# Kernel tuning notes

Hardware: AMD Instinct MI355X
Metric: run time of the kernel (lower is better)

## Reference

```python
import jax, jax.numpy as jnp
import numpy as np

B, LATENT, HID, OUT, SEQ = 256, 512, 1024, 256, 128


def setup_inputs() -> dict:
    key = jax.random.key(0)
    ks = jax.random.split(key, 5)
    s = lambda fan: 1.0 / np.sqrt(fan)
    return {
        "latent": jax.random.normal(ks[0], (B, LATENT), jnp.float32),
        "fc_W": jax.random.normal(ks[1], (HID, LATENT), jnp.float32) * s(LATENT),
        "fc_b": jnp.zeros((HID,), jnp.float32),
        "W_ih": jax.random.normal(ks[2], (4 * HID, OUT), jnp.float32) * s(HID),
        "W_hh": jax.random.normal(ks[3], (4 * HID, HID), jnp.float32) * s(HID),
        "b_ih": jnp.zeros((4 * HID,), jnp.float32),
        "b_hh": jnp.zeros((4 * HID,), jnp.float32),
        "out_W": jax.random.normal(ks[4], (OUT, HID), jnp.float32) * s(HID),
        "out_b": jnp.zeros((OUT,), jnp.float32),
    }


def reference(latent, fc_W, fc_b, W_ih, W_hh, b_ih, b_hh, out_W, out_b):
    # hidden init from latent; cell init zero (num_layers = 1)
    h0 = latent @ fc_W.T + fc_b                       # [B, HID]
    c0 = jnp.zeros_like(h0)
    x0 = jnp.zeros((latent.shape[0], out_W.shape[0]), latent.dtype)  # [B, OUT]
    bias = b_ih + b_hh
    H = h0.shape[-1]

    def step(carry, _):
        x, h, c = carry
        gates = x @ W_ih.T + h @ W_hh.T + bias        # [B, 4H], torch order i,f,g,o
        i = jax.nn.sigmoid(gates[:, 0 * H:1 * H])
        f = jax.nn.sigmoid(gates[:, 1 * H:2 * H])
        g = jnp.tanh(gates[:, 2 * H:3 * H])
        o = jax.nn.sigmoid(gates[:, 3 * H:4 * H])
        c = f * c + i * g
        h = o * jnp.tanh(c)
        y = h @ out_W.T + out_b                        # [B, OUT]; fed back as next input
        return (y, h, c), y

    _, ys = jax.lax.scan(step, (x0, h0, c0), None, length=SEQ)
    return jnp.transpose(ys, (1, 0, 2))               # [B, SEQ, OUT]
```

## Files before the change

### kernel.cpp

```cpp
#include <hip/hip_runtime.h>


typedef __attribute__((ext_vector_type(8))) _Float16 f16x8;
typedef __attribute__((ext_vector_type(4))) float f32x4;
typedef __attribute__((ext_vector_type(4))) unsigned u32x4;

#define MFMA16(a,b,c) __builtin_amdgcn_mfma_f32_16x16x32_f16(a,b,c,0,0,0)

__device__ __forceinline__ short f2h(float x){
  return __builtin_bit_cast(short, (_Float16)x);
}
__device__ __forceinline__ unsigned pack2h(float a, float b){
  unsigned short ua = __builtin_bit_cast(unsigned short, (_Float16)a);
  unsigned short ub = __builtin_bit_cast(unsigned short, (_Float16)b);
  return (unsigned)ua | ((unsigned)ub << 16);
}

__device__ __forceinline__ void gll16(const void* g, void* l){
  __builtin_amdgcn_global_load_lds((const __attribute__((address_space(1))) void*)g,
                                   (__attribute__((address_space(3))) void*)l, 16, 0, 0);
}

__device__ __forceinline__ void stage_t(const short* gRC, int ldk, short* lds, int lane, int wv){
#pragma unroll
  for (int jj = 0; jj < 2; ++jj){
    int j = wv*2 + jj;
    const short* src = gRC + (size_t)(j*8 + (lane>>3))*ldk + ((lane&7)*8);
    gll16(src, lds + j*512);
  }
}

__device__ __forceinline__ f16x8 fragh(const short* t, int r, int kk, int lane){
  int row = r + (lane & 15);
  int k0  = (kk<<5) + ((lane>>4)<<3);
  return *(const f16x8*)(t + row*64 + (k0 ^ ((row & 7)<<3)));
}

template<int CH>
__device__ __forceinline__ void core_k(const short* Ag, const short* Bg, int ldk,
                                       short* As, short* Bs, f32x4 (&acc)[2][2],
                                       int lane, int wv, int wr, int wc){
  stage_t(Ag, ldk, As, lane, wv);
  stage_t(Bg, ldk, Bs, lane, wv);
  __syncthreads();
  int buf = 0;
  for (int c = 0; c < CH; ++c){
    if (c+1 < CH){
      stage_t(Ag + (c+1)*64, ldk, As + (buf^1)*4096, lane, wv);
      stage_t(Bg + (c+1)*64, ldk, Bs + (buf^1)*4096, lane, wv);
    }
    const short* At = As + buf*4096;
    const short* Bt = Bs + buf*4096;
#pragma unroll
    for (int kk = 0; kk < 2; ++kk){
      f16x8 a0 = fragh(At, wr,    kk, lane), a1 = fragh(At, wr+16, kk, lane);
      f16x8 b0 = fragh(Bt, wc,    kk, lane), b1 = fragh(Bt, wc+16, kk, lane);
      acc[0][0] = MFMA16(a0,b0,acc[0][0]); acc[0][1] = MFMA16(a0,b1,acc[0][1]);
      acc[1][0] = MFMA16(a1,b0,acc[1][0]); acc[1][1] = MFMA16(a1,b1,acc[1][1]);
    }
    __syncthreads();
    buf ^= 1;
  }
}


__global__ void k_prep(const float* __restrict__ W_ih, const float* __restrict__ out_W,
                       const float* __restrict__ latent, const float* __restrict__ fc_W,
                       const float* __restrict__ W_hh,
                       const float* __restrict__ b_ih, const float* __restrict__ b_hh,
                       short* __restrict__ WihF, short* __restrict__ owT,
                       short* __restrict__ owB, short* __restrict__ latF,
                       short* __restrict__ fcwF, short* __restrict__ W0F,
                       float* __restrict__ bias0, unsigned* __restrict__ flags){
  int T = blockDim.x*gridDim.x, t0 = blockIdx.x*blockDim.x + threadIdx.x;
  for (int i = t0; i < 8192; i += T) flags[i] = 0u;
  for (int idx = t0; idx < 4096*256; idx += T){
    int r = idx >> 8, j = idx & 255;
    WihF[(size_t)r*256 + (j ^ ((r&7)<<3))] = f2h(W_ih[idx]);
  }
  for (int idx = t0; idx < 1024*256; idx += T){
    int c = idx >> 8, j = idx & 255;
    owT[(size_t)c*256 + (j ^ ((c&7)<<3))] = f2h(out_W[(size_t)j*1024 + c]);
  }
  for (int idx = t0; idx < 256*1024; idx += T){
    int o = idx >> 10, k = idx & 1023;
    owB[(size_t)o*1024 + (k ^ ((o&7)<<3))] = f2h(out_W[idx]);
  }
  for (int idx = t0; idx < 256*512; idx += T){
    int b = idx >> 9, j = idx & 511;
    latF[(size_t)b*512 + (j ^ ((b&7)<<3))] = f2h(latent[idx]);
  }
  for (int idx = t0; idx < 1024*512; idx += T){
    int n = idx >> 9, j = idx & 511;
    fcwF[(size_t)n*512 + (j ^ ((n&7)<<3))] = f2h(fc_W[idx]);
  }
  for (int idx = t0; idx < 4096*1024; idx += T){
    int r = idx >> 10, k = idx & 1023;
    int p = ((r & 1023)<<2) | (r >> 10);
    size_t a = ((size_t)(p>>4)*32 + (k>>5))*512 + ((size_t)((((k>>3)&3)<<4)|(p&15)))*8 + (k&7);
    W0F[a] = f2h(W_hh[idx]);
  }
  for (int r = t0; r < 4096; r += T){
    int rp = ((r & 1023)<<2) | (r >> 10);
    bias0[rp] = b_ih[r] + b_hh[r];
  }
}

__global__ void k_bias1(const float* __restrict__ W_ih, const float* __restrict__ out_b,
                        const float* __restrict__ bias0, float* __restrict__ bias1){
  int r = blockIdx.x*256 + threadIdx.x;
  float s = 0.f;
  for (int j = 0; j < 256; ++j) s += W_ih[(size_t)r*256 + j]*out_b[j];
  int rp = ((r & 1023)<<2) | (r >> 10);
  bias1[rp] = bias0[rp] + s;
}

__global__ __launch_bounds__(256) void k_wtotal(const short* __restrict__ WihF,
                                                const short* __restrict__ owT,
                                                const float* __restrict__ W_hh,
                                                short* __restrict__ WtF){
  __shared__ __align__(16) short As[2*4096];
  __shared__ __align__(16) short Bs[2*4096];
  int tid = threadIdx.x, lane = tid & 63, wv = tid >> 6;
  int wr = (wv>>1)*32, wc = (wv&1)*32;
  int Rm = blockIdx.x*64, Rn = blockIdx.y*64;
  f32x4 acc[2][2] = {};
  core_k<4>(WihF + (size_t)Rm*256, owT + (size_t)Rn*256, 256, As, Bs, acc, lane, wv, wr, wc);
#pragma unroll
  for (int mi = 0; mi < 2; ++mi)
#pragma unroll
  for (int ni = 0; ni < 2; ++ni)
#pragma unroll
  for (int r = 0; r < 4; ++r){
    int row = Rm + wr + mi*16 + ((lane>>4)<<2) + r;
    int col = Rn + wc + ni*16 + (lane & 15);
    float v = acc[mi][ni][r] + W_hh[(size_t)row*1024 + col];
    int p = ((row & 1023)<<2) | (row >> 10);
    size_t a = ((size_t)(p>>4)*32 + (col>>5))*512 + ((size_t)((((col>>3)&3)<<4)|(p&15)))*8 + (col&7);
    WtF[a] = f2h(v);
  }
}

__global__ __launch_bounds__(256) void k_h0(const short* __restrict__ latF,
                                            const short* __restrict__ fcwF,
                                            const float* __restrict__ fc_b,
                                            short* __restrict__ A0){
  __shared__ __align__(16) short As[2*4096];
  __shared__ __align__(16) short Bs[2*4096];
  int tid = threadIdx.x, lane = tid & 63, wv = tid >> 6;
  int wr = (wv>>1)*32, wc = (wv&1)*32;
  int Rm = blockIdx.x*64, Rn = blockIdx.y*64;
  f32x4 acc[2][2] = {};
  core_k<8>(latF + (size_t)Rm*512, fcwF + (size_t)Rn*512, 512, As, Bs, acc, lane, wv, wr, wc);
#pragma unroll
  for (int mi = 0; mi < 2; ++mi)
#pragma unroll
  for (int ni = 0; ni < 2; ++ni)
#pragma unroll
  for (int r = 0; r < 4; ++r){
    int row = Rm + wr + mi*16 + ((lane>>4)<<2) + r;
    int col = Rn + wc + ni*16 + (lane & 15);
    float h = acc[mi][ni][r] + fc_b[col];
    A0[(size_t)row*1024 + (col ^ ((row&7)<<3))] = f2h(h);
  }
}

__global__ __launch_bounds__(512, 1) void k_persist(
    const short* __restrict__ WtF, const short* __restrict__ W0F,
    const float* __restrict__ bias0, const float* __restrict__ bias1,
    short* __restrict__ A0, short* __restrict__ A1, short* __restrict__ Hh,
    unsigned* __restrict__ flags){
  __shared__ __align__(16) short Asl[32*1024];
  __shared__ __align__(16) float Lg0[32*132];
  __shared__ __align__(16) float Lg1[32*132];
  const int tid = threadIdx.x, lane = tid & 63, wv = tid >> 6;
  const int wg = blockIdx.x;
  const int chain = wg & 7, gw = wg >> 3;
  const int wn = wv & 3, kh = wv >> 2;
  const int cbase = gw*8 + wn*2, sbase = kh*16;

  f16x8 Breg[2][16];
  {
    const short* src = WtF + ((size_t)cbase*32 + sbase)*512 + lane*8;
#pragma unroll
    for (int cf = 0; cf < 2; ++cf)
#pragma unroll
      for (int s = 0; s < 16; ++s)
        Breg[cf][s] = *(const f16x8*)(src + (size_t)(cf*32 + s)*512);
  }
  const short* W0base = W0F + ((size_t)cbase*32 + sbase)*512 + lane*8;

  const int r0 = lane & 15;
  const int kql = (lane>>4)<<3;
  const int sw = (r0 & 7) << 3;

  const int er = tid >> 4, up = tid & 15;
  const int grow = chain*32 + er;
  const int swE = (grow & 7) << 3;
  const int posE = (gw*32 + 2*up) ^ swE;
  const f32x4 b1qA = *(const f32x4*)(bias1 + gw*128 + 8*up);
  const f32x4 b1qB = *(const f32x4*)(bias1 + gw*128 + 8*up + 4);
  float cA = 0.f, cB = 0.f;

  unsigned* flagC = flags + (size_t)chain*64;

  for (int t = 0; t < 128; ++t){
    const short* Ain = (t & 1) ? A1 : A0;
    short* Aout = (t & 1) ? A0 : A1;

    {
      u32x4 stg[8];
      const short* base = Ain + (size_t)(chain*32)*1024;
#pragma unroll
      for (int q = 0; q < 8; ++q){
        int i = wv*8 + q;
        const short* src = base + (size_t)(i>>1)*1024 + (i&1)*512 + lane*8;
        asm volatile("global_load_dwordx4 %0, %1, off sc0 sc1"
                     : "=v"(stg[q]) : "v"(src));
      }
      asm volatile("s_waitcnt vmcnt(0)" ::: "memory");
#pragma unroll
      for (int q = 0; q < 8; ++q){
        int i = wv*8 + q;
        *(u32x4*)((char*)Asl + (size_t)i*1024 + (size_t)lane*16) = stg[q];
      }
    }
    __syncthreads();

    f32x4 acc[2][2] = {};
    const short* Ar0 = Asl + r0*1024;
    const short* Ar1 = Asl + (16 + r0)*1024;
    if (t == 0){
#pragma unroll
      for (int s = 0; s < 16; ++s){
        int k = (sbase + s)*32 + kql;
        f16x8 w0 = *(const f16x8*)(W0base + (size_t)(0*32 + s)*512);
        f16x8 w1 = *(const f16x8*)(W0base + (size_t)(1*32 + s)*512);
        f16x8 a0 = *(const f16x8*)(Ar0 + (k ^ sw));
        f16x8 a1 = *(const f16x8*)(Ar1 + (k ^ sw));
        acc[0][0] = MFMA16(a0, w0, acc[0][0]);
        acc[0][1] = MFMA16(a0, w1, acc[0][1]);
        acc[1][0] = MFMA16(a1, w0, acc[1][0]);
        acc[1][1] = MFMA16(a1, w1, acc[1][1]);
      }
    } else {
#pragma unroll
      for (int s = 0; s < 16; ++s){
        int k = (sbase + s)*32 + kql;
        f16x8 a0 = *(const f16x8*)(Ar0 + (k ^ sw));
        f16x8 a1 = *(const f16x8*)(Ar1 + (k ^ sw));
        acc[0][0] = MFMA16(a0, Breg[0][s], acc[0][0]);
        acc[0][1] = MFMA16(a0, Breg[1][s], acc[0][1]);
        acc[1][0] = MFMA16(a1, Breg[0][s], acc[1][0]);
        acc[1][1] = MFMA16(a1, Breg[1][s], acc[1][1]);
      }
    }
    {
      float* Lg = kh ? Lg1 : Lg0;
#pragma unroll
      for (int rf = 0; rf < 2; ++rf)
#pragma unroll
      for (int cf = 0; cf < 2; ++cf)
#pragma unroll
      for (int j = 0; j < 4; ++j)
        Lg[(rf*16 + ((lane>>4)<<2) + j)*132 + wn*32 + cf*16 + r0] = acc[rf][cf][j];
    }
    __syncthreads();
    {
      f32x4 gA = *(const f32x4*)(Lg0 + er*132 + 8*up);
      f32x4 gB = *(const f32x4*)(Lg0 + er*132 + 8*up + 4);
      f32x4 hA = *(const f32x4*)(Lg1 + er*132 + 8*up);
      f32x4 hB = *(const f32x4*)(Lg1 + er*132 + 8*up + 4);
      if (t){ gA = gA + hA + b1qA; gB = gB + hB + b1qB; }
      else {
        gA = gA + hA + *(const f32x4*)(bias0 + gw*128 + 8*up);
        gB = gB + hB + *(const f32x4*)(bias0 + gw*128 + 8*up + 4);
      }
      float I0 = 1.f/(1.f+__expf(-gA[0])), F0 = 1.f/(1.f+__expf(-gA[1]));
      float G0 = tanhf(gA[2]),             O0 = 1.f/(1.f+__expf(-gA[3]));
      float I1 = 1.f/(1.f+__expf(-gB[0])), F1 = 1.f/(1.f+__expf(-gB[1]));
      float G1 = tanhf(gB[2]),             O1 = 1.f/(1.f+__expf(-gB[3]));
      cA = F0*cA + I0*G0;  float h0v = O0*tanhf(cA);
      cB = F1*cB + I1*G1;  float h1v = O1*tanhf(cB);
      unsigned pk = pack2h(h0v, h1v);
      short* pa = Aout + (size_t)grow*1024 + posE;
      asm volatile("global_store_dword %0, %1, off sc0 sc1" :: "v"(pa), "v"(pk));
      *(unsigned*)(Hh + (size_t)t*262144 + (size_t)grow*1024 + posE) = pk;
      asm volatile("s_waitcnt vmcnt(0)" ::: "memory");
    }
    if (t < 127){
      __syncthreads();
      if (tid == 0){
        unsigned val = (unsigned)(t+1);
        unsigned* fp = flagC + gw;
        asm volatile("global_store_dword %0, %1, off sc0 sc1" :: "v"(fp), "v"(val) : "memory");
      }
      if (wv == 0){
        const unsigned* pp = flagC + (size_t)lane*4;
        unsigned tgt = (unsigned)(t+1);
        while (true){
          u32x4 f;
          asm volatile("global_load_dwordx4 %0, %1, off sc0 sc1\n\ts_waitcnt vmcnt(0)"
                       : "=v"(f) : "v"(pp) : "memory");
          bool ok = (lane >= 8) || (f[0] >= tgt && f[1] >= tgt && f[2] >= tgt && f[3] >= tgt);
          if (__all(ok)) break;
        }
      }
      __syncthreads();
    }
  }
}

__global__ __launch_bounds__(512) void k_y(const short* __restrict__ Hh,
                                           const short* __restrict__ owB,
                                           const float* __restrict__ out_b,
                                           float* __restrict__ out){
  __shared__ __align__(16) short As[2*8192];
  __shared__ __align__(16) short Bs[2*16384];
  int tid = threadIdx.x, lane = tid & 63, wv = tid >> 6;
  int wr = (wv>>2)*64, wc = (wv&3)*64;
  size_t Rm = (size_t)blockIdx.x * 128;
  const short* Ab = Hh + Rm*1024;
  f32x4 acc[4][4] = {};
  auto stA = [&](int c, short* dst){
#pragma unroll
    for (int jj = 0; jj < 2; ++jj){ int j = wv*2 + jj;
      gll16(Ab + (size_t)(j*8 + (lane>>3))*1024 + c*64 + (lane&7)*8, dst + j*512); }
  };
  auto stB = [&](int c, short* dst){
#pragma unroll
    for (int jj = 0; jj < 4; ++jj){ int j = wv*4 + jj;
      gll16(owB + (size_t)(j*8 + (lane>>3))*1024 + c*64 + (lane&7)*8, dst + j*512); }
  };
  stA(0, As); stB(0, Bs);
  __syncthreads();
  int buf = 0;
  for (int c = 0; c < 16; ++c){
    if (c+1 < 16){ stA(c+1, As + (buf^1)*8192); stB(c+1, Bs + (buf^1)*16384); }
    const short* At = As + buf*8192;
    const short* Bt = Bs + buf*16384;
#pragma unroll
    for (int kk = 0; kk < 2; ++kk){
      f16x8 av[4], bv[4];
#pragma unroll
      for (int mi = 0; mi < 4; ++mi) av[mi] = fragh(At, wr + mi*16, kk, lane);
#pragma unroll
      for (int ni = 0; ni < 4; ++ni) bv[ni] = fragh(Bt, wc + ni*16, kk, lane);
#pragma unroll
      for (int mi = 0; mi < 4; ++mi)
#pragma unroll
      for (int ni = 0; ni < 4; ++ni) acc[mi][ni] = MFMA16(av[mi], bv[ni], acc[mi][ni]);
    }
    __syncthreads();
    buf ^= 1;
  }
#pragma unroll
  for (int ni = 0; ni < 4; ++ni){
    int col = wc + ni*16 + (lane & 15);
    float bv = out_b[col];
#pragma unroll
    for (int mi = 0; mi < 4; ++mi)
#pragma unroll
    for (int r = 0; r < 4; ++r){
      size_t m = Rm + wr + mi*16 + ((lane>>4)<<2) + r;
      int t = (int)(m >> 8), bb = (int)(m & 255);
      out[(size_t)bb*32768 + (size_t)t*256 + col] = acc[mi][ni][r] + bv;
    }
  }
}

extern "C" void kernel_launch(void* const* d_in, const int* in_sizes, int n_in,
                              void* d_out, int out_size, void* d_ws, size_t ws_size,
                              hipStream_t stream) {
  (void)in_sizes; (void)n_in; (void)out_size; (void)ws_size;
  const float* latent = (const float*)d_in[0];
  const float* fc_W   = (const float*)d_in[1];
  const float* fc_b   = (const float*)d_in[2];
  const float* W_ih   = (const float*)d_in[3];
  const float* W_hh   = (const float*)d_in[4];
  const float* b_ih   = (const float*)d_in[5];
  const float* b_hh   = (const float*)d_in[6];
  const float* out_W  = (const float*)d_in[7];
  const float* out_b  = (const float*)d_in[8];
  float* out = (float*)d_out;
  char*  ws  = (char*)d_ws;
  const size_t MB = 1u << 20;
  short* WtF   = (short*)(ws + 0);
  short* W0F   = (short*)(ws + 8*MB);
  short* A0    = (short*)(ws + 16*MB);
  short* A1    = (short*)(ws + 16*MB + 524288);
  float* bias0 = (float*)(ws + 17*MB);
  float* bias1 = (float*)(ws + 17*MB + 65536);
  short* owB   = (short*)(ws + 17*MB + 131072);
  short* WihF  = (short*)(ws + 18*MB);
  short* owT   = (short*)(ws + 20*MB);
  short* latF  = (short*)(ws + 20*MB + 524288);
  short* fcwF  = (short*)(ws + 21*MB);
  unsigned* flg= (unsigned*)(ws + 22*MB);
  short* Hh    = (short*)(ws + 23*MB);

  k_prep<<<1024, 256, 0, stream>>>(W_ih, out_W, latent, fc_W, W_hh, b_ih, b_hh,
                                   WihF, owT, owB, latF, fcwF, W0F, bias0, flg);
  k_bias1<<<16, 256, 0, stream>>>(W_ih, out_b, bias0, bias1);
  k_wtotal<<<dim3(64,16), 256, 0, stream>>>(WihF, owT, W_hh, WtF);
  k_h0<<<dim3(4,16), 256, 0, stream>>>(latF, fcwF, fc_b, A0);
  k_persist<<<256, 512, 0, stream>>>(WtF, W0F, bias0, bias1, A0, A1, Hh, flg);
  k_y<<<256, 512, 0, stream>>>(Hh, owB, out_b, out);
}
```

Before: 655.1 us.

## Read recurrent state from Hh history and stage it via direct global-to-LDS loads

Drops the A0/A1 ping-pong buffers. Each step now stores h once to the Hh history slice with a coherent store, and the next step reads that slice back, which removes one global store per thread per step. The A-tile staging is switched from register loads plus LDS writes to global_load_lds, and the resident weights are loaded with inline asm after an acquire fence. A risk is coherence: global_load_lds is issued without the sc0/sc1 bits, so it may read stale cached data from other workgroups unless the flag handshake and fence are enough, and no explicit vmcnt wait is visible before the barrier.

```diff
diff --git a/kernel.cpp b/kernel.cpp
--- a/kernel.cpp
+++ b/kernel.cpp
@@ -20,6 +20,8 @@
   __builtin_amdgcn_global_load_lds((const __attribute__((address_space(1))) void*)g,
                                    (__attribute__((address_space(3))) void*)l, 16, 0, 0);
 }
+
+__device__ __forceinline__ void vm0(){ asm volatile("s_waitcnt vmcnt(0)" ::: "memory"); }
 
 __device__ __forceinline__ void stage_t(const short* gRC, int ldk, short* lds, int lane, int wv){
 #pragma unroll
@@ -168,7 +170,7 @@
 __global__ __launch_bounds__(512, 1) void k_persist(
     const short* __restrict__ WtF, const short* __restrict__ W0F,
     const float* __restrict__ bias0, const float* __restrict__ bias1,
-    short* __restrict__ A0, short* __restrict__ A1, short* __restrict__ Hh,
+    const short* __restrict__ A0, short* __restrict__ Hh,
     unsigned* __restrict__ flags){
   __shared__ __align__(16) short Asl[32*1024];
   __shared__ __align__(16) float Lg0[32*132];
@@ -179,14 +181,19 @@
   const int wn = wv & 3, kh = wv >> 2;
   const int cbase = gw*8 + wn*2, sbase = kh*16;
 
-  f16x8 Breg[2][16];
+  __builtin_amdgcn_fence(__ATOMIC_ACQUIRE, "agent");
+
+  u32x4 braw[2][16];
   {
     const short* src = WtF + ((size_t)cbase*32 + sbase)*512 + lane*8;
 #pragma unroll
     for (int cf = 0; cf < 2; ++cf)
 #pragma unroll
-      for (int s = 0; s < 16; ++s)
-        Breg[cf][s] = *(const f16x8*)(src + (size_t)(cf*32 + s)*512);
+      for (int s = 0; s < 16; ++s){
+        const short* p = src + (size_t)(cf*32 + s)*512;
+        asm volatile("global_load_dwordx4 %0, %1, off" : "=v"(braw[cf][s]) : "v"(p));
+      }
+    vm0();
   }
   const short* W0base = W0F + ((size_t)cbase*32 + sbase)*512 + lane*8;
 
@@ -205,24 +212,13 @@
   unsigned* flagC = flags + (size_t)chain*64;
 
   for (int t = 0; t < 128; ++t){
-    const short* Ain = (t & 1) ? A1 : A0;
-    short* Aout = (t & 1) ? A0 : A1;
-
     {
-      u32x4 stg[8];
-      const short* base = Ain + (size_t)(chain*32)*1024;
+      const short* base = (t == 0) ? A0 : (Hh + (size_t)(t-1)*262144);
+      const short* bb = base + (size_t)(chain*32)*1024;
 #pragma unroll
       for (int q = 0; q < 8; ++q){
         int i = wv*8 + q;
-        const short* src = base + (size_t)(i>>1)*1024 + (i&1)*512 + lane*8;
-        asm volatile("global_load_dwordx4 %0, %1, off sc0 sc1"
-                     : "=v"(stg[q]) : "v"(src));
-      }
-      asm volatile("s_waitcnt vmcnt(0)" ::: "memory");
-#pragma unroll
-      for (int q = 0; q < 8; ++q){
-        int i = wv*8 + q;
-        *(u32x4*)((char*)Asl + (size_t)i*1024 + (size_t)lane*16) = stg[q];
+        gll16(bb + (size_t)(i>>1)*1024 + (i&1)*512 + lane*8, Asl + i*512);
       }
     }
     __syncthreads();
@@ -249,10 +245,10 @@
         int k = (sbase + s)*32 + kql;
         f16x8 a0 = *(const f16x8*)(Ar0 + (k ^ sw));
         f16x8 a1 = *(const f16x8*)(Ar1 + (k ^ sw));
-        acc[0][0] = MFMA16(a0, Breg[0][s], acc[0][0]);
-        acc[0][1] = MFMA16(a0, Breg[1][s], acc[0][1]);
-        acc[1][0] = MFMA16(a1, Breg[0][s], acc[1][0]);
-        acc[1][1] = MFMA16(a1, Breg[1][s], acc[1][1]);
+        acc[0][0] = MFMA16(a0, __builtin_bit_cast(f16x8, braw[0][s]), acc[0][0]);
+        acc[0][1] = MFMA16(a0, __builtin_bit_cast(f16x8, braw[1][s]), acc[0][1]);
+        acc[1][0] = MFMA16(a1, __builtin_bit_cast(f16x8, braw[0][s]), acc[1][0]);
+        acc[1][1] = MFMA16(a1, __builtin_bit_cast(f16x8, braw[1][s]), acc[1][1]);
       }
     }
     {
@@ -283,10 +279,9 @@
       cA = F0*cA + I0*G0;  float h0v = O0*tanhf(cA);
       cB = F1*cB + I1*G1;  float h1v = O1*tanhf(cB);
       unsigned pk = pack2h(h0v, h1v);
-      short* pa = Aout + (size_t)grow*1024 + posE;
+      short* pa = Hh + (size_t)t*262144 + (size_t)grow*1024 + posE;
       asm volatile("global_store_dword %0, %1, off sc0 sc1" :: "v"(pa), "v"(pk));
-      *(unsigned*)(Hh + (size_t)t*262144 + (size_t)grow*1024 + posE) = pk;
-      asm volatile("s_waitcnt vmcnt(0)" ::: "memory");
+      vm0();
     }
     if (t < 127){
       __syncthreads();
@@ -388,7 +383,6 @@
   short* WtF   = (short*)(ws + 0);
   short* W0F   = (short*)(ws + 8*MB);
   short* A0    = (short*)(ws + 16*MB);
-  short* A1    = (short*)(ws + 16*MB + 524288);
   float* bias0 = (float*)(ws + 17*MB);
   float* bias1 = (float*)(ws + 17*MB + 65536);
   short* owB   = (short*)(ws + 17*MB + 131072);
@@ -404,6 +398,6 @@
   k_bias1<<<16, 256, 0, stream>>>(W_ih, out_b, bias0, bias1);
   k_wtotal<<<dim3(64,16), 256, 0, stream>>>(WihF, owT, W_hh, WtF);
   k_h0<<<dim3(4,16), 256, 0, stream>>>(latF, fcwF, fc_b, A0);
-  k_persist<<<256, 512, 0, stream>>>(WtF, W0F, bias0, bias1, A0, A1, Hh, flg);
+  k_persist<<<256, 512, 0, stream>>>(WtF, W0F, bias0, bias1, A0, Hh, flg);
   k_y<<<256, 512, 0, stream>>>(Hh, owB, out_b, out);
 }
```

Measured after the change: 656.9 us. About the same (+0.3%).

## Replace flag barrier with poison-value data polling on per-step hidden state

Applied to the files above, without the earlier changes.

Removes the per-step flag store/poll barrier between workgroups in the persistent LSTM kernel. Each step now writes h directly into a per-timestep history buffer that was pre-filled with a NaN poison pattern, and consumers spin on their own input rows until no poison remains. This drops the flag round trip, the extra A0/A1 ping-pong store and two block barriers per step. In exchange the prep kernel must poison 64MB of history each call, and any computed fp16 pair that exactly matches the poison pattern would hang the poll.

```diff
diff --git a/kernel.cpp b/kernel.cpp
--- a/kernel.cpp
+++ b/kernel.cpp
@@ -6,6 +6,7 @@
 typedef __attribute__((ext_vector_type(4))) unsigned u32x4;
 
 #define MFMA16(a,b,c) __builtin_amdgcn_mfma_f32_16x16x32_f16(a,b,c,0,0,0)
+#define HPOISON 0x7E007E00u
 
 __device__ __forceinline__ short f2h(float x){
   return __builtin_bit_cast(short, (_Float16)x);
@@ -20,6 +21,8 @@
   __builtin_amdgcn_global_load_lds((const __attribute__((address_space(1))) void*)g,
                                    (__attribute__((address_space(3))) void*)l, 16, 0, 0);
 }
+
+__device__ __forceinline__ void vm0(){ asm volatile("s_waitcnt vmcnt(0)" ::: "memory"); }
 
 __device__ __forceinline__ void stage_t(const short* gRC, int ldk, short* lds, int lane, int wv){
 #pragma unroll
@@ -71,9 +74,13 @@
                        short* __restrict__ WihF, short* __restrict__ owT,
                        short* __restrict__ owB, short* __restrict__ latF,
                        short* __restrict__ fcwF, short* __restrict__ W0F,
-                       float* __restrict__ bias0, unsigned* __restrict__ flags){
+                       float* __restrict__ bias0, short* __restrict__ Hh){
   int T = blockDim.x*gridDim.x, t0 = blockIdx.x*blockDim.x + threadIdx.x;
-  for (int i = t0; i < 8192; i += T) flags[i] = 0u;
+  {
+    u32x4* Hp = (u32x4*)Hh;
+    const u32x4 P4 = {HPOISON, HPOISON, HPOISON, HPOISON};
+    for (int i = t0; i < 4194304; i += T) Hp[i] = P4;
+  }
   for (int idx = t0; idx < 4096*256; idx += T){
     int r = idx >> 8, j = idx & 255;
     WihF[(size_t)r*256 + (j ^ ((r&7)<<3))] = f2h(W_ih[idx]);
@@ -168,8 +175,7 @@
 __global__ __launch_bounds__(512, 1) void k_persist(
     const short* __restrict__ WtF, const short* __restrict__ W0F,
     const float* __restrict__ bias0, const float* __restrict__ bias1,
-    short* __restrict__ A0, short* __restrict__ A1, short* __restrict__ Hh,
-    unsigned* __restrict__ flags){
+    const short* __restrict__ A0, short* __restrict__ Hh){
   __shared__ __align__(16) short Asl[32*1024];
   __shared__ __align__(16) float Lg0[32*132];
   __shared__ __align__(16) float Lg1[32*132];
@@ -202,23 +208,38 @@
   const f32x4 b1qB = *(const f32x4*)(bias1 + gw*128 + 8*up + 4);
   float cA = 0.f, cB = 0.f;
 
-  unsigned* flagC = flags + (size_t)chain*64;
-
   for (int t = 0; t < 128; ++t){
-    const short* Ain = (t & 1) ? A1 : A0;
-    short* Aout = (t & 1) ? A0 : A1;
-
-    {
-      u32x4 stg[8];
-      const short* base = Ain + (size_t)(chain*32)*1024;
+    if (t == 0){
+      const short* bb = A0 + (size_t)(chain*32)*1024;
 #pragma unroll
       for (int q = 0; q < 8; ++q){
         int i = wv*8 + q;
-        const short* src = base + (size_t)(i>>1)*1024 + (i&1)*512 + lane*8;
-        asm volatile("global_load_dwordx4 %0, %1, off sc0 sc1"
-                     : "=v"(stg[q]) : "v"(src));
+        gll16(bb + (size_t)(i>>1)*1024 + (i&1)*512 + lane*8, Asl + i*512);
       }
-      asm volatile("s_waitcnt vmcnt(0)" ::: "memory");
+    } else {
+      const short* bb = Hh + (size_t)(t-1)*262144 + (size_t)(chain*32)*1024;
+      u32x4 stg[8];
+      unsigned pend = 0xFFu;
+      do {
+#pragma unroll
+        for (int q = 0; q < 8; ++q)
+          if (pend & (1u<<q)){
+            int i = wv*8 + q;
+            const short* src = bb + (size_t)(i>>1)*1024 + (i&1)*512 + lane*8;
+            asm volatile("global_load_dwordx4 %0, %1, off sc0 sc1"
+                         : "=v"(stg[q]) : "v"(src) : "memory");
+          }
+        vm0();
+        unsigned np = 0;
+#pragma unroll
+        for (int q = 0; q < 8; ++q)
+          if (pend & (1u<<q)){
+            bool bad = (stg[q][0] == HPOISON) | (stg[q][1] == HPOISON) |
+                       (stg[q][2] == HPOISON) | (stg[q][3] == HPOISON);
+            if (__any(bad)) np |= 1u<<q;
+          }
+        pend = np;
+      } while (pend);
 #pragma unroll
       for (int q = 0; q < 8; ++q){
         int i = wv*8 + q;
@@ -283,30 +304,8 @@
       cA = F0*cA + I0*G0;  float h0v = O0*tanhf(cA);
       cB = F1*cB + I1*G1;  float h1v = O1*tanhf(cB);
       unsigned pk = pack2h(h0v, h1v);
-      short* pa = Aout + (size_t)grow*1024 + posE;
-      asm volatile("global_store_dword %0, %1, off sc0 sc1" :: "v"(pa), "v"(pk));
-      *(unsigned*)(Hh + (size_t)t*262144 + (size_t)grow*1024 + posE) = pk;
-      asm volatile("s_waitcnt vmcnt(0)" ::: "memory");
-    }
-    if (t < 127){
-      __syncthreads();
-      if (tid == 0){
-        unsigned val = (unsigned)(t+1);
-        unsigned* fp = flagC + gw;
-        asm volatile("global_store_dword %0, %1, off sc0 sc1" :: "v"(fp), "v"(val) : "memory");
-      }
-      if (wv == 0){
-        const unsigned* pp = flagC + (size_t)lane*4;
-        unsigned tgt = (unsigned)(t+1);
-        while (true){
-          u32x4 f;
-          asm volatile("global_load_dwordx4 %0, %1, off sc0 sc1\n\ts_waitcnt vmcnt(0)"
-                       : "=v"(f) : "v"(pp) : "memory");
-          bool ok = (lane >= 8) || (f[0] >= tgt && f[1] >= tgt && f[2] >= tgt && f[3] >= tgt);
-          if (__all(ok)) break;
-        }
-      }
-      __syncthreads();
+      short* pa = Hh + (size_t)t*262144 + (size_t)grow*1024 + posE;
+      asm volatile("global_store_dword %0, %1, off sc0 sc1" :: "v"(pa), "v"(pk) : "memory");
     }
   }
 }
@@ -388,7 +387,6 @@
   short* WtF   = (short*)(ws + 0);
   short* W0F   = (short*)(ws + 8*MB);
   short* A0    = (short*)(ws + 16*MB);
-  short* A1    = (short*)(ws + 16*MB + 524288);
   float* bias0 = (float*)(ws + 17*MB);
   float* bias1 = (float*)(ws + 17*MB + 65536);
   short* owB   = (short*)(ws + 17*MB + 131072);
@@ -396,14 +394,13 @@
   short* owT   = (short*)(ws + 20*MB);
   short* latF  = (short*)(ws + 20*MB + 524288);
   short* fcwF  = (short*)(ws + 21*MB);
-  unsigned* flg= (unsigned*)(ws + 22*MB);
   short* Hh    = (short*)(ws + 23*MB);
 
   k_prep<<<1024, 256, 0, stream>>>(W_ih, out_W, latent, fc_W, W_hh, b_ih, b_hh,
-                                   WihF, owT, owB, latF, fcwF, W0F, bias0, flg);
+                                   WihF, owT, owB, latF, fcwF, W0F, bias0, Hh);
   k_bias1<<<16, 256, 0, stream>>>(W_ih, out_b, bias0, bias1);
   k_wtotal<<<dim3(64,16), 256, 0, stream>>>(WihF, owT, W_hh, WtF);
   k_h0<<<dim3(4,16), 256, 0, stream>>>(latF, fcwF, fc_b, A0);
-  k_persist<<<256, 512, 0, stream>>>(WtF, W0F, bias0, bias1, A0, A1, Hh, flg);
+  k_persist<<<256, 512, 0, stream>>>(WtF, W0F, bias0, bias1, A0, Hh);
   k_y<<<256, 512, 0, stream>>>(Hh, owB, out_b, out);
 }
```

New measurement: 931.1 us. +42.1%, slower.
